# Kernel optimization log

Hardware: AMD Instinct MI355X
Metric: run time of the kernel (lower is better)

## Reference

```python
import jax, jax.numpy as jnp
import numpy as np

DIM = 1024
HEADS = 16
WIN = 128          # local window size
BATCH = 4
SEQ = 4096
HEAD_DIM = DIM // HEADS
HIDDEN = 2 * DIM   # GEGLU hidden_dim = 2*dim
EPS = 1e-5
NEG_INF = -1e9


def layer_norm(x, g, b):
    m = jnp.mean(x, axis=-1, keepdims=True)
    v = jnp.mean((x - m) ** 2, axis=-1, keepdims=True)
    return (x - m) * jax.lax.rsqrt(v + EPS) * g + b


def sliding_causal_local_attn(x, wq, wk, wv, wo, bo, rel_bias):
    # x: [B, S, D]; sliding-window causal attention: each query attends to
    # its own window plus the previous window (look_backward=1), causally masked.
    B, S, D = x.shape
    h, w, dh = HEADS, WIN, HEAD_DIM
    nw = S // w
    scale = dh ** -0.5

    def split_heads(t):  # [B,S,D] -> [B,h,nw,w,dh]
        return t.reshape(B, S, h, dh).transpose(0, 2, 1, 3).reshape(B, h, nw, w, dh)

    q = split_heads(x @ wq)
    k = split_heads(x @ wk)
    v = split_heads(x @ wv)

    # context = [previous window ; current window] -> [B,h,nw,2w,dh]
    k_pad = jnp.pad(k, ((0, 0), (0, 0), (1, 0), (0, 0), (0, 0)))
    v_pad = jnp.pad(v, ((0, 0), (0, 0), (1, 0), (0, 0), (0, 0)))
    kc = jnp.concatenate([k_pad[:, :, :-1], k_pad[:, :, 1:]], axis=3)
    vc = jnp.concatenate([v_pad[:, :, :-1], v_pad[:, :, 1:]], axis=3)

    logits = jnp.einsum('bhnid,bhnjd->bhnij', q, kc) * scale  # [B,h,nw,w,2w]

    i = jnp.arange(w)[:, None]        # query pos within window
    j = jnp.arange(2 * w)[None, :]    # key pos within [prev;cur] context
    dist = i + w - j                  # relative distance, 0..2w-1 when causal
    causal = dist >= 0
    # learned relative position bias per head, indexed by distance
    bias = rel_bias[:, jnp.clip(dist, 0, 2 * w - 1)]  # [h, w, 2w]
    logits = logits + bias[None, :, None]

    n_idx = jnp.arange(nw)[:, None, None]
    valid = causal[None] & ((n_idx > 0) | (j[None] >= w))  # mask padded first window
    logits = jnp.where(valid[None, None], logits, NEG_INF)

    attn = jax.nn.softmax(logits, axis=-1)
    out = jnp.einsum('bhnij,bhnjd->bhnid', attn, vc)           # [B,h,nw,w,dh]
    out = out.reshape(B, h, S, dh).transpose(0, 2, 1, 3).reshape(B, S, D)
    return out @ wo + bo


def geglu(x, w1, b1, w2, b2):
    proj = x @ w1 + b1                         # [B,S,2*HIDDEN]
    val, gate = jnp.split(proj, 2, axis=-1)
    return (val * jax.nn.gelu(gate, approximate=False)) @ w2 + b2


def setup_inputs() -> dict:
    key = jax.random.key(0)
    ks = jax.random.split(key, 12)
    sd = 0.02
    return {
        'x': jax.random.normal(ks[0], (BATCH, SEQ, DIM), jnp.float32),
        'ln1_g': jnp.ones((DIM,), jnp.float32),
        'ln1_b': jnp.zeros((DIM,), jnp.float32),
        'ln2_g': jnp.ones((DIM,), jnp.float32),
        'ln2_b': jnp.zeros((DIM,), jnp.float32),
        'wq': jax.random.normal(ks[1], (DIM, DIM), jnp.float32) * sd,
        'wk': jax.random.normal(ks[2], (DIM, DIM), jnp.float32) * sd,
        'wv': jax.random.normal(ks[3], (DIM, DIM), jnp.float32) * sd,
        'wo': jax.random.normal(ks[4], (DIM, DIM), jnp.float32) * sd,
        'bo': jnp.zeros((DIM,), jnp.float32),
        'rel_bias': jax.random.normal(ks[5], (HEADS, 2 * WIN), jnp.float32) * sd,
        'w_ff1': jax.random.normal(ks[6], (DIM, 2 * HIDDEN), jnp.float32) * sd,
        'b_ff1': jnp.zeros((2 * HIDDEN,), jnp.float32),
        'w_ff2': jax.random.normal(ks[7], (HIDDEN, DIM), jnp.float32) * sd,
        'b_ff2': jnp.zeros((DIM,), jnp.float32),
    }


def reference(x, ln1_g, ln1_b, ln2_g, ln2_b, wq, wk, wv, wo, bo, rel_bias,
              w_ff1, b_ff1, w_ff2, b_ff2):
    x = x + sliding_causal_local_attn(layer_norm(x, ln1_g, ln1_b),
                                      wq, wk, wv, wo, bo, rel_bias)
    x = x + geglu(layer_norm(x, ln2_g, ln2_b), w_ff1, b_ff1, w_ff2, b_ff2)
    return x
```

## Files before the change

kernel.cpp:

```cpp
#include <hip/hip_runtime.h>
#include <math.h>

typedef __attribute__((ext_vector_type(8))) short s16x8;
typedef __attribute__((ext_vector_type(4))) float f32x4;

__device__ __forceinline__ float b2f(unsigned short u){
  unsigned int i = ((unsigned int)u) << 16;
  float f; __builtin_memcpy(&f, &i, 4); return f;
}
__device__ __forceinline__ unsigned short f2b(float f){
  unsigned int i; __builtin_memcpy(&i, &f, 4);
  unsigned int r = (i + 0x7fffu + ((i >> 16) & 1u)) >> 16;
  return (unsigned short)r;
}
__device__ __forceinline__ f32x4 mfma16(s16x8 a, s16x8 b, f32x4 c){
  return __builtin_amdgcn_mfma_f32_16x16x32_bf16(a, b, c, 0, 0, 0);
}
__device__ __forceinline__ float gelu_exact(float x){
  return 0.5f * x * (1.0f + erff(x * 0.70710678118654752f));
}
__device__ __forceinline__ void gl_lds16(const unsigned short* g, unsigned short* l){
  __builtin_amdgcn_global_load_lds(
      (const __attribute__((address_space(1))) unsigned int*)g,
      (__attribute__((address_space(3))) unsigned int*)l, 16, 0, 0);
}

__device__ __forceinline__ void ln_row(const float* __restrict__ xrow,
                                       const float* __restrict__ g,
                                       const float* __restrict__ b,
                                       unsigned short* __restrict__ orow, int lane){
  const float4* xr = (const float4*)xrow;
  float4 u[4];
  #pragma unroll
  for(int q = 0; q < 4; q++) u[q] = xr[lane + 64*q];
  float s = 0.0f, ss = 0.0f;
  #pragma unroll
  for(int q = 0; q < 4; q++){
    s  += u[q].x + u[q].y + u[q].z + u[q].w;
    ss += u[q].x*u[q].x + u[q].y*u[q].y + u[q].z*u[q].z + u[q].w*u[q].w;
  }
  #pragma unroll
  for(int o = 32; o; o >>= 1){ s += __shfl_xor(s, o, 64); ss += __shfl_xor(ss, o, 64); }
  float m = s * (1.0f/1024.0f);
  float inv = rsqrtf(ss * (1.0f/1024.0f) - m*m + 1e-5f);
  #pragma unroll
  for(int q = 0; q < 4; q++){
    float4 ug = ((const float4*)g)[lane + 64*q];
    float4 ub = ((const float4*)b)[lane + 64*q];
    ushort4 o4;
    o4.x = f2b((u[q].x - m) * inv * ug.x + ub.x);
    o4.y = f2b((u[q].y - m) * inv * ug.y + ub.y);
    o4.z = f2b((u[q].z - m) * inv * ug.z + ub.z);
    o4.w = f2b((u[q].w - m) * inv * ug.w + ub.w);
    ((ushort4*)orow)[lane + 64*q] = o4;
  }
}

__global__ __launch_bounds__(256) void prep_k(
    const float* __restrict__ x, const float* __restrict__ ln1_g, const float* __restrict__ ln1_b,
    unsigned short* __restrict__ h,
    const float* __restrict__ wq, const float* __restrict__ wk, const float* __restrict__ wv,
    const float* __restrict__ wo, const float* __restrict__ wff1, const float* __restrict__ wff2,
    unsigned short* __restrict__ wqkvT, unsigned short* __restrict__ woT,
    unsigned short* __restrict__ wff1T, unsigned short* __restrict__ wff2T)
{
  const int bz = blockIdx.x;
  if(bz >= 10240){
    int id = bz - 10240;
    int lane = threadIdx.x & 63, wave = threadIdx.x >> 6;
    int row = id * 4 + wave;
    ln_row(x + (size_t)row*1024, ln1_g, ln1_b, h + (size_t)row*1024, lane);
    return;
  }
  const float* in; unsigned short* out; int R, C, c0, r0;
  if(bz < 4096){
    int w = bz >> 10, id = bz & 1023;
    const float* srcs[4] = {wq, wk, wv, wo};
    unsigned short* dsts[4] = {wqkvT, wqkvT + 1048576, wqkvT + 2097152, woT};
    in = srcs[w]; out = dsts[w]; R = 1024; C = 1024;
    c0 = (id & 31) * 32; r0 = (id >> 5) * 32;
  } else if(bz < 8192){
    int id = bz - 4096;
    in = wff1; out = wff1T; R = 1024; C = 4096;
    c0 = (id & 127) * 32; r0 = (id >> 7) * 32;
  } else {
    int id = bz - 8192;
    in = wff2; out = wff2T; R = 2048; C = 1024;
    c0 = (id & 31) * 32; r0 = (id >> 5) * 32;
  }
  __shared__ unsigned short tile[32][33];
  int tx = threadIdx.x & 31, ty = threadIdx.x >> 5;
  #pragma unroll
  for(int i = 0; i < 4; i++)
    tile[ty + 8*i][tx] = f2b(in[(size_t)(r0 + ty + 8*i) * C + c0 + tx]);
  __syncthreads();
  #pragma unroll
  for(int i = 0; i < 4; i++)
    out[(size_t)(c0 + ty + 8*i) * R + r0 + tx] = tile[tx][ty + 8*i];
}

__global__ __launch_bounds__(256) void ln2_k(const float* __restrict__ x,
                                             const float* __restrict__ g,
                                             const float* __restrict__ b,
                                             unsigned short* __restrict__ out){
  int lane = threadIdx.x & 63, wave = threadIdx.x >> 6;
  int row = blockIdx.x * 4 + wave;
  ln_row(x + (size_t)row*1024, g, b, out + (size_t)row*1024, lane);
}

__global__ __launch_bounds__(256) void gemm_bt(
    const unsigned short* __restrict__ A, const unsigned short* __restrict__ Bt,
    void* Cv, void* Cv2, int N, int n_split, int K,
    const float* __restrict__ bias, const float* res, int c_fp32)
{
  __shared__ __align__(16) unsigned short As[128 * 64];
  __shared__ __align__(16) unsigned short Bs[128 * 64];

  int m_tile, n_tile;
  {
    unsigned int lin = blockIdx.y * gridDim.x + blockIdx.x;
    unsigned int mt = gridDim.y;
    unsigned int xcd = lin & 7u, idx = lin >> 3, mpx = mt >> 3;
    m_tile = xcd * mpx + (idx % mpx);
    n_tile = idx / mpx;
  }
  const int m0 = m_tile * 128, n0 = n_tile * 128;
  const int tid = threadIdx.x;
  const int wave = tid >> 6, lane = tid & 63;
  const int wm = (wave >> 1) * 64, wn = (wave & 1) * 64;
  const int lrow = lane & 15, quad = lane >> 4;

  const int tr  = tid >> 3;
  const int scg = ((tid & 7) ^ (tr & 7)) * 8;
  const int xw  = lrow & 7;

  f32x4 acc[4][4];
  #pragma unroll
  for(int i = 0; i < 4; i++)
    #pragma unroll
    for(int j = 0; j < 4; j++)
      #pragma unroll
      for(int r = 0; r < 4; r++) acc[i][j][r] = 0.0f;

  const int nk = K >> 6;
  for(int kt = 0; kt < nk; kt++){
    const int k0 = kt << 6;
    if(kt) __syncthreads();
    #pragma unroll
    for(int i = 0; i < 4; i++){
      int row = i*32 + tr;
      gl_lds16(&A [(size_t)(m0 + row)*K + k0 + scg], &As[i*2048 + wave*512]);
      gl_lds16(&Bt[(size_t)(n0 + row)*K + k0 + scg], &Bs[i*2048 + wave*512]);
    }
    __syncthreads();
    #pragma unroll
    for(int kk = 0; kk < 2; kk++){
      s16x8 af[4], bfv[4];
      #pragma unroll
      for(int i = 0; i < 4; i++){
        int ga = ((kk<<2) + quad) ^ xw;
        af [i] = *(const s16x8*)&As[(wm + i*16 + lrow)*64 + ga*8];
        bfv[i] = *(const s16x8*)&Bs[(wn + i*16 + lrow)*64 + ga*8];
      }
      #pragma unroll
      for(int i = 0; i < 4; i++)
        #pragma unroll
        for(int j = 0; j < 4; j++)
          acc[i][j] = mfma16(af[i], bfv[j], acc[i][j]);
    }
  }
  const int qr = quad * 4;
  #pragma unroll
  for(int i = 0; i < 4; i++){
    #pragma unroll
    for(int j = 0; j < 4; j++){
      int col = n0 + wn + j*16 + lrow;
      float bv = bias ? bias[col] : 0.0f;
      #pragma unroll
      for(int r = 0; r < 4; r++){
        int row = m0 + wm + i*16 + qr + r;
        float v = acc[i][j][r] + bv;
        if(col < n_split){
          size_t idx = (size_t)row * n_split + col;
          if(res) v += res[idx];
          if(c_fp32) ((float*)Cv)[idx] = v;
          else       ((unsigned short*)Cv)[idx] = f2b(v);
        } else {
          size_t idx = (size_t)row * (N - n_split) + (col - n_split);
          ((unsigned short*)Cv2)[idx] = f2b(v);
        }
      }
    }
  }
}

__global__ __launch_bounds__(256) void geglu_gemm(
    const unsigned short* __restrict__ A, const unsigned short* __restrict__ Bt,
    unsigned short* __restrict__ C, int K,
    const float* __restrict__ bias)
{
  __shared__ __align__(16) unsigned short pool[2 * 128 * 64];
  unsigned short* As = pool;
  unsigned short* Bs = pool + 128*64;

  int m_tile, n_tile;
  {
    unsigned int lin = blockIdx.y * gridDim.x + blockIdx.x;
    unsigned int mt = gridDim.y;
    unsigned int xcd = lin & 7u, idx = lin >> 3, mpx = mt >> 3;
    m_tile = xcd * mpx + (idx % mpx);
    n_tile = idx / mpx;
  }
  const int m0 = m_tile * 128, nv0 = n_tile * 64;
  const int tid = threadIdx.x;
  const int wave = tid >> 6, lane = tid & 63;
  const int wm = (wave >> 1) * 64, wn = (wave & 1) * 64;
  const int lrow = lane & 15, quad = lane >> 4;

  const int tr  = tid >> 3;
  const int scg = ((tid & 7) ^ (tr & 7)) * 8;
  const int xw  = lrow & 7;

  f32x4 acc[4][4];
  #pragma unroll
  for(int i = 0; i < 4; i++)
    #pragma unroll
    for(int j = 0; j < 4; j++)
      #pragma unroll
      for(int r = 0; r < 4; r++) acc[i][j][r] = 0.0f;

  const int nk = K >> 6;
  for(int kt = 0; kt < nk; kt++){
    const int k0 = kt << 6;
    if(kt) __syncthreads();
    #pragma unroll
    for(int i = 0; i < 4; i++){
      int row = i*32 + tr;
      int brow = (row < 64) ? (nv0 + row) : (2048 + nv0 + row - 64);
      gl_lds16(&A [(size_t)(m0 + row)*K + k0 + scg], &As[i*2048 + wave*512]);
      gl_lds16(&Bt[(size_t)brow     *K + k0 + scg], &Bs[i*2048 + wave*512]);
    }
    __syncthreads();
    #pragma unroll
    for(int kk = 0; kk < 2; kk++){
      s16x8 af[4], bfv[4];
      #pragma unroll
      for(int i = 0; i < 4; i++){
        int ga = ((kk<<2) + quad) ^ xw;
        af [i] = *(const s16x8*)&As[(wm + i*16 + lrow)*64 + ga*8];
        bfv[i] = *(const s16x8*)&Bs[(wn + i*16 + lrow)*64 + ga*8];
      }
      #pragma unroll
      for(int i = 0; i < 4; i++)
        #pragma unroll
        for(int j = 0; j < 4; j++)
          acc[i][j] = mfma16(af[i], bfv[j], acc[i][j]);
    }
  }
  __syncthreads();
  float* gS = (float*)pool;
  const int qr = quad * 4;
  if(wn == 64){
    #pragma unroll
    for(int i = 0; i < 4; i++)
      #pragma unroll
      for(int j = 0; j < 4; j++){
        int cl = j*16 + lrow;
        float bv = bias[2048 + nv0 + cl];
        #pragma unroll
        for(int r = 0; r < 4; r++)
          gS[(wm + i*16 + qr + r)*64 + cl] = gelu_exact(acc[i][j][r] + bv);
      }
  }
  __syncthreads();
  if(wn == 0){
    #pragma unroll
    for(int i = 0; i < 4; i++)
      #pragma unroll
      for(int j = 0; j < 4; j++){
        int cl = j*16 + lrow;
        float bv = bias[nv0 + cl];
        #pragma unroll
        for(int r = 0; r < 4; r++){
          int rl = wm + i*16 + qr + r;
          float v = (acc[i][j][r] + bv) * gS[rl*64 + cl];
          C[(size_t)(m0 + rl) * 2048 + nv0 + cl] = f2b(v);
        }
      }
  }
}

__global__ __launch_bounds__(256, 1) void attn_k(const unsigned short* __restrict__ qk,
                                                 const unsigned short* __restrict__ vbuf,
                                                 const float* __restrict__ rel_bias,
                                                 unsigned short* __restrict__ attn_out)
{
  __shared__ unsigned short kvS[128 * 72];
  __shared__ unsigned short PS[128 * 136];
  __shared__ float biasS[256];

  const int n = blockIdx.x, h = blockIdx.y, b = blockIdx.z;
  const int tid = threadIdx.x;
  const int wave = tid >> 6, lane = tid & 63;
  const int lrow = lane & 15, quad = lane >> 4, lk = quad * 8;
  const int rbase = wave * 32;
  const size_t rowbase = (size_t)b * 4096;
  const int prev = (n > 0) ? (n - 1) : 0;

  biasS[tid] = rel_bias[h * 256 + tid];

  s16x8 aq[2][2];
  #pragma unroll
  for(int mi = 0; mi < 2; mi++)
    #pragma unroll
    for(int kk = 0; kk < 2; kk++)
      aq[mi][kk] = *(const s16x8*)&qk[(rowbase + n*128 + rbase + mi*16 + lrow)*2048
                                      + h*64 + kk*32 + lk];

  f32x4 lg[2][16];
  #pragma unroll
  for(int mi = 0; mi < 2; mi++)
    #pragma unroll
    for(int nj = 0; nj < 16; nj++)
      #pragma unroll
      for(int r = 0; r < 4; r++) lg[mi][nj][r] = 0.0f;

  for(int jh = 0; jh < 2; jh++){
    if(jh) __syncthreads();
    #pragma unroll
    for(int it = 0; it < 4; it++){
      int cid = tid + it * 256;
      int jloc = cid >> 3, c8 = (cid & 7) * 8;
      int j = jh * 128 + jloc;
      int srow = (j < 128) ? (prev*128 + j) : (n*128 + j - 128);
      *(s16x8*)&kvS[jloc*72 + c8] =
        *(const s16x8*)&qk[(rowbase + srow)*2048 + 1024 + h*64 + c8];
    }
    __syncthreads();
    #pragma unroll
    for(int njl = 0; njl < 8; njl++){
      #pragma unroll
      for(int kk = 0; kk < 2; kk++){
        s16x8 bk = *(const s16x8*)&kvS[(njl*16 + lrow)*72 + kk*32 + lk];
        #pragma unroll
        for(int mi = 0; mi < 2; mi++)
          lg[mi][jh*8 + njl] = mfma16(aq[mi][kk], bk, lg[mi][jh*8 + njl]);
      }
    }
  }
  __syncthreads();

  #pragma unroll
  for(int mi = 0; mi < 2; mi++){
    #pragma unroll
    for(int r = 0; r < 4; r++){
      int i = rbase + mi*16 + quad*4 + r;
      float mx = -3e38f;
      #pragma unroll
      for(int nj = 0; nj < 16; nj++){
        int j = nj*16 + lrow;
        int dist = i + 128 - j;
        bool valid = (dist >= 0) && ((n > 0) || (j >= 128));
        float l = valid ? (lg[mi][nj][r] * 0.125f + biasS[dist & 255]) : -1e9f;
        lg[mi][nj][r] = l;
        mx = fmaxf(mx, l);
      }
      #pragma unroll
      for(int o = 1; o < 16; o <<= 1) mx = fmaxf(mx, __shfl_xor(mx, o, 64));
      float s = 0.0f;
      #pragma unroll
      for(int nj = 0; nj < 16; nj++){
        float p = __expf(lg[mi][nj][r] - mx);
        lg[mi][nj][r] = p;
        s += p;
      }
      #pragma unroll
      for(int o = 1; o < 16; o <<= 1) s += __shfl_xor(s, o, 64);
      float inv = 1.0f / s;
      #pragma unroll
      for(int nj = 0; nj < 16; nj++) lg[mi][nj][r] *= inv;
    }
  }

  f32x4 o_acc[2][4];
  #pragma unroll
  for(int mi = 0; mi < 2; mi++)
    #pragma unroll
    for(int nj = 0; nj < 4; nj++)
      #pragma unroll
      for(int r = 0; r < 4; r++) o_acc[mi][nj][r] = 0.0f;

  for(int jh = 0; jh < 2; jh++){
    {
      int jloc = tid >> 1;
      int dbase = (tid & 1) * 32;
      int j = jh * 128 + jloc;
      int srow = (j < 128) ? (prev*128 + j) : (n*128 + j - 128);
      const unsigned short* vr = &vbuf[(rowbase + srow)*1024 + h*64 + dbase];
      #pragma unroll
      for(int i8 = 0; i8 < 4; i8++){
        s16x8 vv = *(const s16x8*)&vr[i8 * 8];
        #pragma unroll
        for(int e = 0; e < 8; e++)
          kvS[(dbase + i8*8 + e)*136 + jloc] = (unsigned short)vv[e];
      }
    }
    #pragma unroll
    for(int mi = 0; mi < 2; mi++)
      #pragma unroll
      for(int r = 0; r < 4; r++)
        #pragma unroll
        for(int njl = 0; njl < 8; njl++)
          PS[(rbase + mi*16 + quad*4 + r)*136 + njl*16 + lrow] = f2b(lg[mi][jh*8 + njl][r]);
    __syncthreads();
    #pragma unroll
    for(int kk = 0; kk < 4; kk++){
      s16x8 ap[2];
      #pragma unroll
      for(int mi = 0; mi < 2; mi++)
        ap[mi] = *(const s16x8*)&PS[(rbase + mi*16 + lrow)*136 + kk*32 + lk];
      #pragma unroll
      for(int nj = 0; nj < 4; nj++){
        s16x8 bv = *(const s16x8*)&kvS[(nj*16 + lrow)*136 + kk*32 + lk];
        #pragma unroll
        for(int mi = 0; mi < 2; mi++)
          o_acc[mi][nj] = mfma16(ap[mi], bv, o_acc[mi][nj]);
      }
    }
    __syncthreads();
  }

  #pragma unroll
  for(int mi = 0; mi < 2; mi++)
    #pragma unroll
    for(int nj = 0; nj < 4; nj++)
      #pragma unroll
      for(int r = 0; r < 4; r++){
        size_t row = rowbase + n*128 + rbase + mi*16 + quad*4 + r;
        int col = h*64 + nj*16 + lrow;
        attn_out[row * 1024 + col] = f2b(o_acc[mi][nj][r]);
      }
}

extern "C" void kernel_launch(void* const* d_in, const int* in_sizes, int n_in,
                              void* d_out, int out_size, void* d_ws, size_t ws_size,
                              hipStream_t stream) {
  const float* x     = (const float*)d_in[0];
  const float* ln1_g = (const float*)d_in[1];
  const float* ln1_b = (const float*)d_in[2];
  const float* ln2_g = (const float*)d_in[3];
  const float* ln2_b = (const float*)d_in[4];
  const float* wq    = (const float*)d_in[5];
  const float* wk    = (const float*)d_in[6];
  const float* wv    = (const float*)d_in[7];
  const float* wo    = (const float*)d_in[8];
  const float* bo    = (const float*)d_in[9];
  const float* rel   = (const float*)d_in[10];
  const float* wff1  = (const float*)d_in[11];
  const float* bff1  = (const float*)d_in[12];
  const float* wff2  = (const float*)d_in[13];
  const float* bff2  = (const float*)d_in[14];
  float* out = (float*)d_out;
  char*  ws  = (char*)d_ws;

  unsigned short* wqkvT = (unsigned short*)(ws);
  unsigned short* woT   = (unsigned short*)(ws +  6291456);
  unsigned short* wff1T = (unsigned short*)(ws +  8388608);
  unsigned short* wff2T = (unsigned short*)(ws + 16777216);
  unsigned short* h     = (unsigned short*)(ws + 20971520);
  unsigned short* qk    = (unsigned short*)(ws + 54525952);
  unsigned short* ff    = qk;
  unsigned short* vbuf  = (unsigned short*)d_out;
  float*          x1    = out;

  prep_k<<<14336, 256, 0, stream>>>(x, ln1_g, ln1_b, h,
                                    wq, wk, wv, wo, wff1, wff2,
                                    wqkvT, woT, wff1T, wff2T);
  gemm_bt<<<dim3(24, 128), 256, 0, stream>>>(h, wqkvT, qk, vbuf, 3072, 2048, 1024,
                                             nullptr, nullptr, 0);
  attn_k<<<dim3(32, 16, 4), 256, 0, stream>>>(qk, vbuf, rel, h);
  gemm_bt<<<dim3(8, 128), 256, 0, stream>>>(h, woT, x1, nullptr, 1024, 1024, 1024,
                                            bo, x, 1);
  ln2_k<<<4096, 256, 0, stream>>>(x1, ln2_g, ln2_b, h);
  geglu_gemm<<<dim3(32, 128), 256, 0, stream>>>(h, wff1T, ff, 1024, bff1);
  gemm_bt<<<dim3(8, 128), 256, 0, stream>>>(ff, wff2T, out, nullptr, 1024, 1024, 2048,
                                            bff2, x1, 1);
}
```

Measured before the change: 867.0 us.

## Replace GEMMs with 256x256-tile double-buffered 8-wave kernel with interleaved prefetch

Replaces the 128x128 single-buffered GEMM and separate GEGLU GEMM with one templated 256-row tile kernel using 512 threads, double-buffered LDS, and direct-to-LDS prefetch of the next K tile staged between MFMA groups, with s_setprio around the MFMA bursts. The GEGLU variant interleaves value and gate rows in 16-row groups, so each wave holds matching value/gate accumulators and fuses the gelu product in registers without an LDS round trip. The aim is to hide global-load latency and raise data reuse per byte loaded. In exchange it uses more LDS and registers (one block per CU), and launches fewer, larger blocks, which can leave CUs underfilled.

```diff
diff --git a/kernel.cpp b/kernel.cpp
--- a/kernel.cpp
+++ b/kernel.cpp
@@ -108,183 +108,186 @@
   ln_row(x + (size_t)row*1024, g, b, out + (size_t)row*1024, lane);
 }
 
-__global__ __launch_bounds__(256) void gemm_bt(
+template<int MODE>
+__global__ __launch_bounds__(512, 1) void gemm256(
     const unsigned short* __restrict__ A, const unsigned short* __restrict__ Bt,
     void* Cv, void* Cv2, int N, int n_split, int K,
-    const float* __restrict__ bias, const float* res, int c_fp32)
+    const float* __restrict__ bias, const float* __restrict__ res)
 {
-  __shared__ __align__(16) unsigned short As[128 * 64];
-  __shared__ __align__(16) unsigned short Bs[128 * 64];
+  __shared__ __align__(16) unsigned short As[2][256*64];
+  __shared__ __align__(16) unsigned short Bs[2][256*64];
 
   int m_tile, n_tile;
   {
     unsigned int lin = blockIdx.y * gridDim.x + blockIdx.x;
-    unsigned int mt = gridDim.y;
-    unsigned int xcd = lin & 7u, idx = lin >> 3, mpx = mt >> 3;
+    unsigned int mpx = gridDim.y >> 3;
+    unsigned int xcd = lin & 7u, idx = lin >> 3;
     m_tile = xcd * mpx + (idx % mpx);
     n_tile = idx / mpx;
   }
-  const int m0 = m_tile * 128, n0 = n_tile * 128;
+  const int m0 = m_tile * 256;
+  const int n0 = n_tile * (MODE == 1 ? 128 : 256);
   const int tid = threadIdx.x;
   const int wave = tid >> 6, lane = tid & 63;
-  const int wm = (wave >> 1) * 64, wn = (wave & 1) * 64;
-  const int lrow = lane & 15, quad = lane >> 4;
-
-  const int tr  = tid >> 3;
-  const int scg = ((tid & 7) ^ (tr & 7)) * 8;
-  const int xw  = lrow & 7;
-
-  f32x4 acc[4][4];
-  #pragma unroll
-  for(int i = 0; i < 4; i++)
+  const int ln3 = lane >> 3;
+  const int cg  = (lane & 7) ^ ln3;
+  const int wm = (wave >> 2) * 128, wn = (wave & 3) * 64;
+  const int lrow = lane & 15, quad = lane >> 4, xw = lrow & 7;
+
+  const unsigned short* aSrc[4];
+  const unsigned short* bSrc[4];
+  #pragma unroll
+  for(int hq = 0; hq < 4; hq++){
+    int rt = hq*64 + wave*8 + ln3;
+    aSrc[hq] = A + (size_t)(m0 + rt)*K + cg*8;
+    int brow;
+    if(MODE == 1){
+      int grp = rt >> 4;
+      brow = (grp & 1)*2048 + n0 + ((grp >> 1)*16) + (rt & 15);
+    } else {
+      brow = n0 + rt;
+    }
+    bSrc[hq] = Bt + (size_t)brow*K + cg*8;
+  }
+
+#define STAGE_A(bsel, hh, koff) do{ \
+    gl_lds16(aSrc[(hh)*2+0] + (koff), &As[(bsel)][(hh)*8192 + wave*512]); \
+    gl_lds16(aSrc[(hh)*2+1] + (koff), &As[(bsel)][(hh)*8192 + 4096 + wave*512]); }while(0)
+#define STAGE_B(bsel, hh, koff) do{ \
+    gl_lds16(bSrc[(hh)*2+0] + (koff), &Bs[(bsel)][(hh)*8192 + wave*512]); \
+    gl_lds16(bSrc[(hh)*2+1] + (koff), &Bs[(bsel)][(hh)*8192 + 4096 + wave*512]); }while(0)
+#define RD(buf, rowbase, kk) \
+    (*(const s16x8*)&(buf)[((rowbase) + lrow)*64 + (((((kk)<<2)+quad)^xw)*8)])
+
+  f32x4 acc[8][4];
+  #pragma unroll
+  for(int i = 0; i < 8; i++)
     #pragma unroll
     for(int j = 0; j < 4; j++)
       #pragma unroll
       for(int r = 0; r < 4; r++) acc[i][j][r] = 0.0f;
 
+  STAGE_A(0,0,0); STAGE_A(0,1,0); STAGE_B(0,0,0); STAGE_B(0,1,0);
+
+  s16x8 af[4][2], bf[4][2];
   const int nk = K >> 6;
+  #pragma unroll 2
   for(int kt = 0; kt < nk; kt++){
-    const int k0 = kt << 6;
-    if(kt) __syncthreads();
-    #pragma unroll
-    for(int i = 0; i < 4; i++){
-      int row = i*32 + tr;
-      gl_lds16(&A [(size_t)(m0 + row)*K + k0 + scg], &As[i*2048 + wave*512]);
-      gl_lds16(&Bt[(size_t)(n0 + row)*K + k0 + scg], &Bs[i*2048 + wave*512]);
-    }
-    __syncthreads();
-    #pragma unroll
-    for(int kk = 0; kk < 2; kk++){
-      s16x8 af[4], bfv[4];
-      #pragma unroll
-      for(int i = 0; i < 4; i++){
-        int ga = ((kk<<2) + quad) ^ xw;
-        af [i] = *(const s16x8*)&As[(wm + i*16 + lrow)*64 + ga*8];
-        bfv[i] = *(const s16x8*)&Bs[(wn + i*16 + lrow)*64 + ga*8];
-      }
-      #pragma unroll
-      for(int i = 0; i < 4; i++)
-        #pragma unroll
-        for(int j = 0; j < 4; j++)
-          acc[i][j] = mfma16(af[i], bfv[j], acc[i][j]);
-    }
-  }
+    const int cur = kt & 1, nxt = cur ^ 1;
+    const int koff = (kt + 1) << 6;
+    const bool pf = (kt + 1 < nk);
+
+    if(pf){ STAGE_A(nxt, 0, koff);
+            asm volatile("s_waitcnt vmcnt(2)\n\ts_barrier" ::: "memory"); }
+    else  { asm volatile("s_waitcnt vmcnt(0)\n\ts_barrier" ::: "memory"); }
+    #pragma unroll
+    for(int i = 0; i < 4; i++){ af[i][0] = RD(As[cur], wm + i*16, 0);
+                                af[i][1] = RD(As[cur], wm + i*16, 1); }
+    #pragma unroll
+    for(int j = 0; j < 2; j++){ bf[j][0] = RD(Bs[cur], wn + j*16, 0);
+                                bf[j][1] = RD(Bs[cur], wn + j*16, 1); }
+    __builtin_amdgcn_s_setprio(1);
+    #pragma unroll
+    for(int i = 0; i < 4; i++)
+      #pragma unroll
+      for(int j = 0; j < 2; j++){
+        acc[i][j] = mfma16(af[i][0], bf[j][0], acc[i][j]);
+        acc[i][j] = mfma16(af[i][1], bf[j][1], acc[i][j]);
+      }
+    __builtin_amdgcn_s_setprio(0);
+
+    if(pf) STAGE_A(nxt, 1, koff);
+    #pragma unroll
+    for(int j = 2; j < 4; j++){ bf[j][0] = RD(Bs[cur], wn + j*16, 0);
+                                bf[j][1] = RD(Bs[cur], wn + j*16, 1); }
+    __builtin_amdgcn_s_setprio(1);
+    #pragma unroll
+    for(int i = 0; i < 4; i++)
+      #pragma unroll
+      for(int j = 2; j < 4; j++){
+        acc[i][j] = mfma16(af[i][0], bf[j][0], acc[i][j]);
+        acc[i][j] = mfma16(af[i][1], bf[j][1], acc[i][j]);
+      }
+    __builtin_amdgcn_s_setprio(0);
+
+    if(pf) STAGE_B(nxt, 0, koff);
+    #pragma unroll
+    for(int i = 0; i < 4; i++){ af[i][0] = RD(As[cur], wm + 64 + i*16, 0);
+                                af[i][1] = RD(As[cur], wm + 64 + i*16, 1); }
+    __builtin_amdgcn_s_setprio(1);
+    #pragma unroll
+    for(int i = 0; i < 4; i++)
+      #pragma unroll
+      for(int j = 0; j < 2; j++){
+        acc[4+i][j] = mfma16(af[i][0], bf[j][0], acc[4+i][j]);
+        acc[4+i][j] = mfma16(af[i][1], bf[j][1], acc[4+i][j]);
+      }
+    __builtin_amdgcn_s_setprio(0);
+
+    if(pf) STAGE_B(nxt, 1, koff);
+    __builtin_amdgcn_s_setprio(1);
+    #pragma unroll
+    for(int i = 0; i < 4; i++)
+      #pragma unroll
+      for(int j = 2; j < 4; j++){
+        acc[4+i][j] = mfma16(af[i][0], bf[j][0], acc[4+i][j]);
+        acc[4+i][j] = mfma16(af[i][1], bf[j][1], acc[4+i][j]);
+      }
+    __builtin_amdgcn_s_setprio(0);
+    asm volatile("s_waitcnt lgkmcnt(0)\n\ts_barrier" ::: "memory");
+  }
+#undef STAGE_A
+#undef STAGE_B
+#undef RD
+
   const int qr = quad * 4;
-  #pragma unroll
-  for(int i = 0; i < 4; i++){
-    #pragma unroll
-    for(int j = 0; j < 4; j++){
-      int col = n0 + wn + j*16 + lrow;
-      float bv = bias ? bias[col] : 0.0f;
-      #pragma unroll
-      for(int r = 0; r < 4; r++){
-        int row = m0 + wm + i*16 + qr + r;
-        float v = acc[i][j][r] + bv;
-        if(col < n_split){
-          size_t idx = (size_t)row * n_split + col;
-          if(res) v += res[idx];
-          if(c_fp32) ((float*)Cv)[idx] = v;
-          else       ((unsigned short*)Cv)[idx] = f2b(v);
-        } else {
-          size_t idx = (size_t)row * (N - n_split) + (col - n_split);
-          ((unsigned short*)Cv2)[idx] = f2b(v);
+  if(MODE == 1){
+    unsigned short* C = (unsigned short*)Cv;
+    const int a4 = wave & 3;
+    #pragma unroll
+    for(int i = 0; i < 8; i++){
+      #pragma unroll
+      for(int gp = 0; gp < 2; gp++){
+        int colv = n0 + a4*32 + gp*16 + lrow;
+        float bv = bias[colv];
+        float bg = bias[2048 + colv];
+        #pragma unroll
+        for(int r = 0; r < 4; r++){
+          size_t row = (size_t)(m0 + wm + i*16 + qr + r);
+          float v  = acc[i][2*gp  ][r] + bv;
+          float gt = acc[i][2*gp+1][r] + bg;
+          C[row*2048 + colv] = f2b(v * gelu_exact(gt));
         }
       }
     }
-  }
-}
-
-__global__ __launch_bounds__(256) void geglu_gemm(
-    const unsigned short* __restrict__ A, const unsigned short* __restrict__ Bt,
-    unsigned short* __restrict__ C, int K,
-    const float* __restrict__ bias)
-{
-  __shared__ __align__(16) unsigned short pool[2 * 128 * 64];
-  unsigned short* As = pool;
-  unsigned short* Bs = pool + 128*64;
-
-  int m_tile, n_tile;
-  {
-    unsigned int lin = blockIdx.y * gridDim.x + blockIdx.x;
-    unsigned int mt = gridDim.y;
-    unsigned int xcd = lin & 7u, idx = lin >> 3, mpx = mt >> 3;
-    m_tile = xcd * mpx + (idx % mpx);
-    n_tile = idx / mpx;
-  }
-  const int m0 = m_tile * 128, nv0 = n_tile * 64;
-  const int tid = threadIdx.x;
-  const int wave = tid >> 6, lane = tid & 63;
-  const int wm = (wave >> 1) * 64, wn = (wave & 1) * 64;
-  const int lrow = lane & 15, quad = lane >> 4;
-
-  const int tr  = tid >> 3;
-  const int scg = ((tid & 7) ^ (tr & 7)) * 8;
-  const int xw  = lrow & 7;
-
-  f32x4 acc[4][4];
-  #pragma unroll
-  for(int i = 0; i < 4; i++)
-    #pragma unroll
-    for(int j = 0; j < 4; j++)
-      #pragma unroll
-      for(int r = 0; r < 4; r++) acc[i][j][r] = 0.0f;
-
-  const int nk = K >> 6;
-  for(int kt = 0; kt < nk; kt++){
-    const int k0 = kt << 6;
-    if(kt) __syncthreads();
-    #pragma unroll
-    for(int i = 0; i < 4; i++){
-      int row = i*32 + tr;
-      int brow = (row < 64) ? (nv0 + row) : (2048 + nv0 + row - 64);
-      gl_lds16(&A [(size_t)(m0 + row)*K + k0 + scg], &As[i*2048 + wave*512]);
-      gl_lds16(&Bt[(size_t)brow     *K + k0 + scg], &Bs[i*2048 + wave*512]);
-    }
-    __syncthreads();
-    #pragma unroll
-    for(int kk = 0; kk < 2; kk++){
-      s16x8 af[4], bfv[4];
-      #pragma unroll
-      for(int i = 0; i < 4; i++){
-        int ga = ((kk<<2) + quad) ^ xw;
-        af [i] = *(const s16x8*)&As[(wm + i*16 + lrow)*64 + ga*8];
-        bfv[i] = *(const s16x8*)&Bs[(wn + i*16 + lrow)*64 + ga*8];
-      }
-      #pragma unroll
-      for(int i = 0; i < 4; i++)
-        #pragma unroll
-        for(int j = 0; j < 4; j++)
-          acc[i][j] = mfma16(af[i], bfv[j], acc[i][j]);
-    }
-  }
-  __syncthreads();
-  float* gS = (float*)pool;
-  const int qr = quad * 4;
-  if(wn == 64){
-    #pragma unroll
-    for(int i = 0; i < 4; i++)
+  } else if(MODE == 0){
+    unsigned short* C1 = (unsigned short*)Cv;
+    unsigned short* C2 = (unsigned short*)Cv2;
+    #pragma unroll
+    for(int i = 0; i < 8; i++)
       #pragma unroll
       for(int j = 0; j < 4; j++){
-        int cl = j*16 + lrow;
-        float bv = bias[2048 + nv0 + cl];
-        #pragma unroll
-        for(int r = 0; r < 4; r++)
-          gS[(wm + i*16 + qr + r)*64 + cl] = gelu_exact(acc[i][j][r] + bv);
-      }
-  }
-  __syncthreads();
-  if(wn == 0){
-    #pragma unroll
-    for(int i = 0; i < 4; i++)
+        int col = n0 + wn + j*16 + lrow;
+        #pragma unroll
+        for(int r = 0; r < 4; r++){
+          size_t row = (size_t)(m0 + wm + i*16 + qr + r);
+          if(col < n_split) C1[row*n_split + col] = f2b(acc[i][j][r]);
+          else              C2[row*(N - n_split) + (col - n_split)] = f2b(acc[i][j][r]);
+        }
+      }
+  } else {
+    float* C = (float*)Cv;
+    #pragma unroll
+    for(int i = 0; i < 8; i++)
       #pragma unroll
       for(int j = 0; j < 4; j++){
-        int cl = j*16 + lrow;
-        float bv = bias[nv0 + cl];
+        int col = n0 + wn + j*16 + lrow;
+        float bv = bias[col];
         #pragma unroll
         for(int r = 0; r < 4; r++){
-          int rl = wm + i*16 + qr + r;
-          float v = (acc[i][j][r] + bv) * gS[rl*64 + cl];
-          C[(size_t)(m0 + rl) * 2048 + nv0 + cl] = f2b(v);
+          size_t row = (size_t)(m0 + wm + i*16 + qr + r);
+          size_t idx = row * (size_t)N + col;
+          C[idx] = acc[i][j][r] + bv + res[idx];
         }
       }
   }
@@ -476,13 +479,14 @@
   prep_k<<<14336, 256, 0, stream>>>(x, ln1_g, ln1_b, h,
                                     wq, wk, wv, wo, wff1, wff2,
                                     wqkvT, woT, wff1T, wff2T);
-  gemm_bt<<<dim3(24, 128), 256, 0, stream>>>(h, wqkvT, qk, vbuf, 3072, 2048, 1024,
-                                             nullptr, nullptr, 0);
+  gemm256<0><<<dim3(12, 64), 512, 0, stream>>>(h, wqkvT, qk, vbuf, 3072, 2048, 1024,
+                                               nullptr, nullptr);
   attn_k<<<dim3(32, 16, 4), 256, 0, stream>>>(qk, vbuf, rel, h);
-  gemm_bt<<<dim3(8, 128), 256, 0, stream>>>(h, woT, x1, nullptr, 1024, 1024, 1024,
-                                            bo, x, 1);
+  gemm256<2><<<dim3(4, 64), 512, 0, stream>>>(h, woT, x1, nullptr, 1024, 0, 1024,
+                                              bo, x);
   ln2_k<<<4096, 256, 0, stream>>>(x1, ln2_g, ln2_b, h);
-  geglu_gemm<<<dim3(32, 128), 256, 0, stream>>>(h, wff1T, ff, 1024, bff1);
-  gemm_bt<<<dim3(8, 128), 256, 0, stream>>>(ff, wff2T, out, nullptr, 1024, 1024, 2048,
-                                            bff2, x1, 1);
-}
+  gemm256<1><<<dim3(16, 64), 512, 0, stream>>>(h, wff1T, ff, nullptr, 2048, 0, 1024,
+                                               bff1, nullptr);
+  gemm256<2><<<dim3(4, 64), 512, 0, stream>>>(ff, wff2T, out, nullptr, 1024, 0, 2048,
+                                              bff2, x1);
+}
```

Result: faster. 730.9 us (-15.7%).
